# Performance work log

Measured on AMD Instinct MI355X. Metric: run time of the kernel, lower is better.

Reference implementation:

```python
import jax, jax.numpy as jnp
import numpy as np

N = 4096          # nodes per graph
F_IN = 256        # node_feature_dim
D_OUT = 128       # out_dim
E = N * N // 2    # edges per graph (so E1+E2 == N*N, required by .view(N, N))
NEG_SLOPE = 0.2   # PyG GATConv default negative_slope


def setup_inputs() -> dict:
    key = jax.random.key(0)
    k = jax.random.split(key, 7)
    x1 = jax.random.normal(k[0], (N, F_IN), dtype=jnp.float32)
    x2 = jax.random.normal(k[1], (N, F_IN), dtype=jnp.float32)
    edge_index1 = jax.random.randint(k[2], (2, E), 0, N, dtype=jnp.int64)
    edge_index2 = jax.random.randint(k[3], (2, E), 0, N, dtype=jnp.int64)
    W = jax.random.normal(k[4], (F_IN, D_OUT), dtype=jnp.float32) * 0.05
    att_src = jax.random.normal(k[5], (D_OUT,), dtype=jnp.float32) * 0.1
    att_dst = jax.random.normal(k[6], (D_OUT,), dtype=jnp.float32) * 0.1
    return {"x1": x1, "x2": x2, "edge_index1": edge_index1,
            "edge_index2": edge_index2, "W": W,
            "att_src": att_src, "att_dst": att_dst}


def reference(x1, x2, edge_index1, edge_index2, W, att_src, att_dst):
    n = x1.shape[0]
    # combine the two graphs into one block-diagonal graph (graph2 node ids shifted)
    x = jnp.concatenate([x1, x2], axis=0)                       # [2N, F]
    ei = jnp.concatenate([edge_index1, edge_index2 + n], axis=1)  # [2, N*N]
    src, dst = ei[0], ei[1]

    # GATConv (heads=1): linear transform then per-node logit halves
    h = x @ W                    # [2N, D]
    a_s = h @ att_src            # [2N]
    a_d = h @ att_dst            # [2N]

    # per-edge attention logits with leaky-relu
    e = jax.nn.leaky_relu(a_s[src] + a_d[dst], NEG_SLOPE)       # [N*N]

    # numerically-stable segment softmax grouped by destination node
    num_seg = 2 * n
    seg_max = jax.ops.segment_max(e, dst, num_segments=num_seg)
    ex = jnp.exp(e - seg_max[dst])
    denom = jax.ops.segment_sum(ex, dst, num_segments=num_seg)
    alpha = ex / denom[dst]                                     # [N*N]

    # forward returns only the attention weights reshaped to [N, N]
    return alpha.reshape(n, n)
```

## Files before the change

kernel.cpp:

```cpp
#include <hip/hip_runtime.h>


#define NNODES 4096
#define NSEG   8192
#define NEG_SLOPE 0.2f
#define EPB 32768

__global__ void k1_wvec(const float* __restrict__ W,
                        const float* __restrict__ att_src,
                        const float* __restrict__ att_dst,
                        float* __restrict__ wvs, float* __restrict__ wvd) {
    int f = threadIdx.x;
    const float* row = W + f * 128;
    float s = 0.f, d = 0.f;
    #pragma unroll 8
    for (int j = 0; j < 128; ++j) {
        float w = row[j];
        s += w * att_src[j];
        d += w * att_dst[j];
    }
    wvs[f] = s; wvd[f] = d;
}

__global__ void k2_logits(const float* __restrict__ x1, const float* __restrict__ x2,
                          const float* __restrict__ wvs, const float* __restrict__ wvd,
                          float* __restrict__ a_s, float* __restrict__ a_d) {
    int wave = blockIdx.x * 4 + (threadIdx.x >> 6);
    int lane = threadIdx.x & 63;
    const float* xrow = (wave < NNODES) ? (x1 + (size_t)wave * 256)
                                        : (x2 + (size_t)(wave - NNODES) * 256);
    float4 xv  = ((const float4*)xrow)[lane];
    float4 wsv = ((const float4*)wvs)[lane];
    float4 wdv = ((const float4*)wvd)[lane];
    float ps = xv.x*wsv.x + xv.y*wsv.y + xv.z*wsv.z + xv.w*wsv.w;
    float pd = xv.x*wdv.x + xv.y*wdv.y + xv.z*wdv.z + xv.w*wdv.w;
    #pragma unroll
    for (int o = 32; o > 0; o >>= 1) {
        ps += __shfl_down(ps, o);
        pd += __shfl_down(pd, o);
    }
    if (lane == 0) { a_s[wave] = ps; a_d[wave] = pd; }
}

__device__ __forceinline__ float lrelu_exp(float e) {
    e = (e > 0.f) ? e : NEG_SLOPE * e;
    return __expf(e);
}

__global__ __launch_bounds__(1024) void k3_denom(
        const int* __restrict__ ei1, const int* __restrict__ ei2,
        const float* __restrict__ a_s, const float* __restrict__ a_d,
        float* __restrict__ partials, int E1, int g1_blocks) {
    __shared__ float ssum[NNODES];
    __shared__ float las[NNODES];
    __shared__ float lad[NNODES];
    int t = threadIdx.x;
    int b = blockIdx.x;
    const int *sp, *dp; int nodeoff, qbase;
    if (b < g1_blocks) { sp = ei1; dp = ei1 + E1; nodeoff = 0;      qbase = b * (EPB/4); }
    else               { sp = ei2; dp = ei2 + E1; nodeoff = NNODES; qbase = (b - g1_blocks) * (EPB/4); }

    ((float4*)las)[t] = ((const float4*)(a_s + nodeoff))[t];
    ((float4*)lad)[t] = ((const float4*)(a_d + nodeoff))[t];
    for (int i = t; i < NNODES; i += 1024) ssum[i] = 0.f;
    __syncthreads();

    const int4* s4 = (const int4*)sp;
    const int4* d4 = (const int4*)dp;
    #pragma unroll
    for (int k = 0; k < 8; ++k) {
        int q = qbase + (k << 10) + t;
        int4 sv = s4[q];
        int4 dv = d4[q];
        float e0 = lrelu_exp(las[sv.x] + lad[dv.x]);
        float e1 = lrelu_exp(las[sv.y] + lad[dv.y]);
        float e2 = lrelu_exp(las[sv.z] + lad[dv.z]);
        float e3 = lrelu_exp(las[sv.w] + lad[dv.w]);
        atomicAdd(&ssum[dv.x], e0);
        atomicAdd(&ssum[dv.y], e1);
        atomicAdd(&ssum[dv.z], e2);
        atomicAdd(&ssum[dv.w], e3);
    }
    __syncthreads();
    float* pb = partials + (size_t)b * NNODES;
    for (int i = t; i < NNODES; i += 1024) pb[i] = ssum[i];
}

__global__ void k4a_reduce(const float* __restrict__ partials,
                           float* __restrict__ partials2, int g1_blocks) {
    int tid = blockIdx.x * blockDim.x + threadIdx.x;
    int c  = tid >> 13;
    int sg = tid & (NSEG - 1);
    int bpc = g1_blocks >> 3;
    int b0 = ((sg < NNODES) ? 0 : g1_blocks) + c * bpc;
    int col = sg & (NNODES - 1);
    float s = 0.f;
    for (int j = 0; j < bpc; ++j)
        s += partials[(size_t)(b0 + j) * NNODES + col];
    partials2[tid] = s;
}

__global__ void k4b_inv(const float* __restrict__ partials2,
                        float* __restrict__ inv_denom) {
    int sg = blockIdx.x * blockDim.x + threadIdx.x;
    float s = 0.f;
    #pragma unroll
    for (int c = 0; c < 8; ++c) s += partials2[c * NSEG + sg];
    inv_denom[sg] = 1.0f / s;
}

__global__ __launch_bounds__(1024) void k5_alpha(
        const int* __restrict__ ei1, const int* __restrict__ ei2,
        const float* __restrict__ a_s, const float* __restrict__ a_d,
        const float* __restrict__ inv_denom,
        float* __restrict__ out, int E1, int g1_blocks) {
    __shared__ float las[NNODES];
    __shared__ float lad[NNODES];
    __shared__ float linv[NNODES];
    int t = threadIdx.x;
    int b = blockIdx.x;
    const int *sp, *dp; int nodeoff, qbase, outbase;
    if (b < g1_blocks) { sp = ei1; dp = ei1 + E1; nodeoff = 0;      qbase = b * (EPB/4); outbase = 0; }
    else               { sp = ei2; dp = ei2 + E1; nodeoff = NNODES; qbase = (b - g1_blocks) * (EPB/4); outbase = E1 / 4; }

    ((float4*)las)[t]  = ((const float4*)(a_s + nodeoff))[t];
    ((float4*)lad)[t]  = ((const float4*)(a_d + nodeoff))[t];
    ((float4*)linv)[t] = ((const float4*)(inv_denom + nodeoff))[t];
    __syncthreads();

    const int4* s4 = (const int4*)sp;
    const int4* d4 = (const int4*)dp;
    float4* out4 = (float4*)out;
    #pragma unroll
    for (int k = 0; k < 8; ++k) {
        int q = qbase + (k << 10) + t;
        int4 sv = s4[q];
        int4 dv = d4[q];
        float4 r;
        r.x = lrelu_exp(las[sv.x] + lad[dv.x]) * linv[dv.x];
        r.y = lrelu_exp(las[sv.y] + lad[dv.y]) * linv[dv.y];
        r.z = lrelu_exp(las[sv.z] + lad[dv.z]) * linv[dv.z];
        r.w = lrelu_exp(las[sv.w] + lad[dv.w]) * linv[dv.w];
        out4[outbase + q] = r;
    }
}

extern "C" void kernel_launch(void* const* d_in, const int* in_sizes, int n_in,
                              void* d_out, int out_size, void* d_ws, size_t ws_size,
                              hipStream_t stream) {
    const float* x1      = (const float*)d_in[0];
    const float* x2      = (const float*)d_in[1];
    const int*   ei1     = (const int*)d_in[2];
    const int*   ei2     = (const int*)d_in[3];
    const float* W       = (const float*)d_in[4];
    const float* att_src = (const float*)d_in[5];
    const float* att_dst = (const float*)d_in[6];
    float* out = (float*)d_out;

    const int E1 = in_sizes[2] / 2;

    float* wsf       = (float*)d_ws;
    float* wvs       = wsf;
    float* wvd       = wsf + 256;
    float* a_s       = wsf + 512;
    float* a_d       = wsf + 512 + NSEG;
    float* inv_denom = wsf + 512 + 2*NSEG;
    float* partials2 = wsf + 32768;
    float* partials  = wsf + 131072;

    hipLaunchKernelGGL(k1_wvec, dim3(1), dim3(256), 0, stream,
                       W, att_src, att_dst, wvs, wvd);
    hipLaunchKernelGGL(k2_logits, dim3(2 * NNODES / 4), dim3(256), 0, stream,
                       x1, x2, wvs, wvd, a_s, a_d);

    int g1_blocks = E1 / EPB;
    hipLaunchKernelGGL(k3_denom, dim3(2 * g1_blocks), dim3(1024), 0, stream,
                       ei1, ei2, a_s, a_d, partials, E1, g1_blocks);
    hipLaunchKernelGGL(k4a_reduce, dim3(8 * NSEG / 256), dim3(256), 0, stream,
                       partials, partials2, g1_blocks);
    hipLaunchKernelGGL(k4b_inv, dim3(NSEG / 256), dim3(256), 0, stream,
                       partials2, inv_denom);

    hipLaunchKernelGGL(k5_alpha, dim3(2 * g1_blocks), dim3(1024), 0, stream,
                       ei1, ei2, a_s, a_d, inv_denom, out, E1, g1_blocks);
}
```

Baseline: 276.8 us.

## Replace LDS atomics with per-wave bins and tag-based conflict resolution

The denominator kernel now gives each wave its own private shared-memory histogram. Instead of LDS float atomics it writes a lane tag, and the lane that wins the tag does a plain add; after 8 retry rounds it falls back to an atomic. Both edge kernels also get smaller thread blocks and register double-buffered prefetch of the int4 edge indices. The aim is to avoid atomic contention and to hide global-load latency. In exchange, k3 now needs about 112KB of LDS per 256-thread block, which sharply limits occupancy, and each insert costs several extra LDS operations.

```diff
diff --git a/kernel.cpp b/kernel.cpp
--- a/kernel.cpp
+++ b/kernel.cpp
@@ -4,7 +4,11 @@
 #define NNODES 4096
 #define NSEG   8192
 #define NEG_SLOPE 0.2f
-#define EPB 32768
+
+#define K3_TPB 256
+#define K3_QPB 8192
+#define K5_TPB 512
+#define K5_QPB 8192
 
 __global__ void k1_wvec(const float* __restrict__ W,
                         const float* __restrict__ att_src,
@@ -47,43 +51,98 @@
     return __expf(e);
 }
 
-__global__ __launch_bounds__(1024) void k3_denom(
+__global__ __launch_bounds__(K3_TPB) void k3_denom(
         const int* __restrict__ ei1, const int* __restrict__ ei2,
         const float* __restrict__ a_s, const float* __restrict__ a_d,
         float* __restrict__ partials, int E1, int g1_blocks) {
-    __shared__ float ssum[NNODES];
+    __shared__ float bins[4][NNODES];
+    __shared__ int   tag[NNODES];
     __shared__ float las[NNODES];
     __shared__ float lad[NNODES];
+    volatile int* vtag = tag;
+
     int t = threadIdx.x;
+    float* binw = bins[t >> 6];
+
     int b = blockIdx.x;
-    const int *sp, *dp; int nodeoff, qbase;
-    if (b < g1_blocks) { sp = ei1; dp = ei1 + E1; nodeoff = 0;      qbase = b * (EPB/4); }
-    else               { sp = ei2; dp = ei2 + E1; nodeoff = NNODES; qbase = (b - g1_blocks) * (EPB/4); }
-
-    ((float4*)las)[t] = ((const float4*)(a_s + nodeoff))[t];
-    ((float4*)lad)[t] = ((const float4*)(a_d + nodeoff))[t];
-    for (int i = t; i < NNODES; i += 1024) ssum[i] = 0.f;
+    const int* sp; int qbase, nodeoff;
+    if (b < g1_blocks) { sp = ei1; qbase = b * K3_QPB; nodeoff = 0; }
+    else               { sp = ei2; qbase = (b - g1_blocks) * K3_QPB; nodeoff = NNODES; }
+    const int4* s4 = (const int4*)sp;
+    const int4* d4 = (const int4*)(sp + E1);
+
+    #pragma unroll
+    for (int i = 0; i < 4; ++i) {
+        ((float4*)las)[t + i*K3_TPB] = ((const float4*)(a_s + nodeoff))[t + i*K3_TPB];
+        ((float4*)lad)[t + i*K3_TPB] = ((const float4*)(a_d + nodeoff))[t + i*K3_TPB];
+    }
+    #pragma unroll
+    for (int i = 0; i < 16; ++i)
+        ((float4*)&bins[0][0])[t + i*K3_TPB] = make_float4(0.f,0.f,0.f,0.f);
     __syncthreads();
 
-    const int4* s4 = (const int4*)sp;
-    const int4* d4 = (const int4*)dp;
-    #pragma unroll
-    for (int k = 0; k < 8; ++k) {
-        int q = qbase + (k << 10) + t;
-        int4 sv = s4[q];
-        int4 dv = d4[q];
-        float e0 = lrelu_exp(las[sv.x] + lad[dv.x]);
-        float e1 = lrelu_exp(las[sv.y] + lad[dv.y]);
-        float e2 = lrelu_exp(las[sv.z] + lad[dv.z]);
-        float e3 = lrelu_exp(las[sv.w] + lad[dv.w]);
-        atomicAdd(&ssum[dv.x], e0);
-        atomicAdd(&ssum[dv.y], e1);
-        atomicAdd(&ssum[dv.z], e2);
-        atomicAdd(&ssum[dv.w], e3);
+    auto insert = [&](int d, float val) {
+        bool pending = true;
+        int rounds = 0;
+        while (__any(pending)) {
+            if (++rounds > 8) {
+                if (pending) atomicAdd(&binw[d], val);
+                break;
+            }
+            if (pending) vtag[d] = t;
+            if (pending && vtag[d] == t) {
+                binw[d] += val;
+                pending = false;
+            }
+        }
+    };
+
+    int4 sbuf[2][4], dbuf[2][4];
+    #pragma unroll
+    for (int i = 0; i < 4; ++i) {
+        int q = qbase + i*K3_TPB + t;
+        sbuf[0][i] = s4[q]; dbuf[0][i] = d4[q];
+    }
+    #pragma unroll
+    for (int bt = 0; bt < 8; ++bt) {
+        int cur = bt & 1, nxt = cur ^ 1;
+        if (bt < 7) {
+            #pragma unroll
+            for (int i = 0; i < 4; ++i) {
+                int q = qbase + ((bt+1)*4 + i)*K3_TPB + t;
+                sbuf[nxt][i] = s4[q]; dbuf[nxt][i] = d4[q];
+            }
+        }
+        #pragma unroll
+        for (int i = 0; i < 4; ++i) {
+            int4 sv = sbuf[cur][i], dv = dbuf[cur][i];
+            float e0 = las[sv.x] + lad[dv.x];
+            float e1 = las[sv.y] + lad[dv.y];
+            float e2 = las[sv.z] + lad[dv.z];
+            float e3 = las[sv.w] + lad[dv.w];
+            float v0 = lrelu_exp(e0), v1 = lrelu_exp(e1);
+            float v2 = lrelu_exp(e2), v3 = lrelu_exp(e3);
+            insert(dv.x, v0); insert(dv.y, v1);
+            insert(dv.z, v2); insert(dv.w, v3);
+        }
     }
     __syncthreads();
+
     float* pb = partials + (size_t)b * NNODES;
-    for (int i = t; i < NNODES; i += 1024) pb[i] = ssum[i];
+    #pragma unroll
+    for (int i = 0; i < 4; ++i) {
+        int c = t + i*K3_TPB;
+        float4 s0 = ((float4*)bins[0])[c];
+        float4 s1 = ((float4*)bins[1])[c];
+        float4 s2 = ((float4*)bins[2])[c];
+        float4 s3 = ((float4*)bins[3])[c];
+        float4 r;
+        r.x = s0.x+s1.x+s2.x+s3.x;
+        r.y = s0.y+s1.y+s2.y+s3.y;
+        r.z = s0.z+s1.z+s2.z+s3.z;
+        r.w = s0.w+s1.w+s2.w+s3.w;
+        ((float4*)pb)[c] = r;
+    }
 }
 
 __global__ void k4a_reduce(const float* __restrict__ partials,
@@ -109,7 +168,7 @@
     inv_denom[sg] = 1.0f / s;
 }
 
-__global__ __launch_bounds__(1024) void k5_alpha(
+__global__ __launch_bounds__(K5_TPB) void k5_alpha(
         const int* __restrict__ ei1, const int* __restrict__ ei2,
         const float* __restrict__ a_s, const float* __restrict__ a_d,
         const float* __restrict__ inv_denom,
@@ -119,29 +178,47 @@
     __shared__ float linv[NNODES];
     int t = threadIdx.x;
     int b = blockIdx.x;
-    const int *sp, *dp; int nodeoff, qbase, outbase;
-    if (b < g1_blocks) { sp = ei1; dp = ei1 + E1; nodeoff = 0;      qbase = b * (EPB/4); outbase = 0; }
-    else               { sp = ei2; dp = ei2 + E1; nodeoff = NNODES; qbase = (b - g1_blocks) * (EPB/4); outbase = E1 / 4; }
-
-    ((float4*)las)[t]  = ((const float4*)(a_s + nodeoff))[t];
-    ((float4*)lad)[t]  = ((const float4*)(a_d + nodeoff))[t];
-    ((float4*)linv)[t] = ((const float4*)(inv_denom + nodeoff))[t];
+    const int* sp; int qbase, outq, nodeoff;
+    if (b < g1_blocks) { sp = ei1; qbase = b * K5_QPB; outq = qbase; nodeoff = 0; }
+    else { sp = ei2; qbase = (b - g1_blocks) * K5_QPB; outq = E1/4 + qbase; nodeoff = NNODES; }
+    const int4* s4 = (const int4*)sp;
+    const int4* d4 = (const int4*)(sp + E1);
+
+    #pragma unroll
+    for (int i = 0; i < 2; ++i) {
+        ((float4*)las)[t + i*K5_TPB]  = ((const float4*)(a_s + nodeoff))[t + i*K5_TPB];
+        ((float4*)lad)[t + i*K5_TPB]  = ((const float4*)(a_d + nodeoff))[t + i*K5_TPB];
+        ((float4*)linv)[t + i*K5_TPB] = ((const float4*)(inv_denom + nodeoff))[t + i*K5_TPB];
+    }
     __syncthreads();
 
-    const int4* s4 = (const int4*)sp;
-    const int4* d4 = (const int4*)dp;
     float4* out4 = (float4*)out;
-    #pragma unroll
-    for (int k = 0; k < 8; ++k) {
-        int q = qbase + (k << 10) + t;
-        int4 sv = s4[q];
-        int4 dv = d4[q];
-        float4 r;
-        r.x = lrelu_exp(las[sv.x] + lad[dv.x]) * linv[dv.x];
-        r.y = lrelu_exp(las[sv.y] + lad[dv.y]) * linv[dv.y];
-        r.z = lrelu_exp(las[sv.z] + lad[dv.z]) * linv[dv.z];
-        r.w = lrelu_exp(las[sv.w] + lad[dv.w]) * linv[dv.w];
-        out4[outbase + q] = r;
+    int4 sbuf[2][4], dbuf[2][4];
+    #pragma unroll
+    for (int i = 0; i < 4; ++i) {
+        int q = qbase + i*K5_TPB + t;
+        sbuf[0][i] = s4[q]; dbuf[0][i] = d4[q];
+    }
+    #pragma unroll
+    for (int bt = 0; bt < 4; ++bt) {
+        int cur = bt & 1, nxt = cur ^ 1;
+        if (bt < 3) {
+            #pragma unroll
+            for (int i = 0; i < 4; ++i) {
+                int q = qbase + ((bt+1)*4 + i)*K5_TPB + t;
+                sbuf[nxt][i] = s4[q]; dbuf[nxt][i] = d4[q];
+            }
+        }
+        #pragma unroll
+        for (int i = 0; i < 4; ++i) {
+            int4 sv = sbuf[cur][i], dv = dbuf[cur][i];
+            float4 r;
+            r.x = lrelu_exp(las[sv.x] + lad[dv.x]) * linv[dv.x];
+            r.y = lrelu_exp(las[sv.y] + lad[dv.y]) * linv[dv.y];
+            r.z = lrelu_exp(las[sv.z] + lad[dv.z]) * linv[dv.z];
+            r.w = lrelu_exp(las[sv.w] + lad[dv.w]) * linv[dv.w];
+            out4[outq + (bt*4 + i)*K5_TPB + t] = r;
+        }
     }
 }
 
@@ -173,14 +250,15 @@
     hipLaunchKernelGGL(k2_logits, dim3(2 * NNODES / 4), dim3(256), 0, stream,
                        x1, x2, wvs, wvd, a_s, a_d);
 
-    int g1_blocks = E1 / EPB;
-    hipLaunchKernelGGL(k3_denom, dim3(2 * g1_blocks), dim3(1024), 0, stream,
-                       ei1, ei2, a_s, a_d, partials, E1, g1_blocks);
+    int g1b3 = (E1 / 4) / K3_QPB;
+    hipLaunchKernelGGL(k3_denom, dim3(2 * g1b3), dim3(K3_TPB), 0, stream,
+                       ei1, ei2, a_s, a_d, partials, E1, g1b3);
     hipLaunchKernelGGL(k4a_reduce, dim3(8 * NSEG / 256), dim3(256), 0, stream,
-                       partials, partials2, g1_blocks);
+                       partials, partials2, g1b3);
     hipLaunchKernelGGL(k4b_inv, dim3(NSEG / 256), dim3(256), 0, stream,
                        partials2, inv_denom);
 
-    hipLaunchKernelGGL(k5_alpha, dim3(2 * g1_blocks), dim3(1024), 0, stream,
-                       ei1, ei2, a_s, a_d, inv_denom, out, E1, g1_blocks);
-}
+    int g1b5 = (E1 / 4) / K5_QPB;
+    hipLaunchKernelGGL(k5_alpha, dim3(2 * g1b5), dim3(K5_TPB), 0, stream,
+                       ei1, ei2, a_s, a_d, inv_denom, out, E1, g1b5);
+}
```

New measurement: 298.5 us. 7.8% more time.

## Store exp values in denom pass and rescale them in alpha pass

Applied to the files above, without the earlier changes.

The denominator kernel now writes the unnormalized exp values straight into the output buffer. The alpha kernel then only reads dst indices and those stored values and multiplies by the inverse denominator. This drops the src index read and the exp recompute from the second pass, at the cost of an extra output write plus read of the same size. The a_d table is now read from global memory instead of being staged in shared memory, which shrinks LDS use per block.

```diff
diff --git a/kernel.cpp b/kernel.cpp
--- a/kernel.cpp
+++ b/kernel.cpp
@@ -4,7 +4,8 @@
 #define NNODES 4096
 #define NSEG   8192
 #define NEG_SLOPE 0.2f
-#define EPB 32768
+#define EK_TPB 1024
+#define EK_QPB 8192
 
 __global__ void k1_wvec(const float* __restrict__ W,
                         const float* __restrict__ att_src,
@@ -47,43 +48,46 @@
     return __expf(e);
 }
 
-__global__ __launch_bounds__(1024) void k3_denom(
+__global__ __launch_bounds__(EK_TPB) void k3_denom(
         const int* __restrict__ ei1, const int* __restrict__ ei2,
         const float* __restrict__ a_s, const float* __restrict__ a_d,
-        float* __restrict__ partials, int E1, int g1_blocks) {
+        float* __restrict__ partials, float* __restrict__ out,
+        int E1, int g1_blocks) {
     __shared__ float ssum[NNODES];
     __shared__ float las[NNODES];
-    __shared__ float lad[NNODES];
     int t = threadIdx.x;
     int b = blockIdx.x;
-    const int *sp, *dp; int nodeoff, qbase;
-    if (b < g1_blocks) { sp = ei1; dp = ei1 + E1; nodeoff = 0;      qbase = b * (EPB/4); }
-    else               { sp = ei2; dp = ei2 + E1; nodeoff = NNODES; qbase = (b - g1_blocks) * (EPB/4); }
+    const int* sp; int qbase, nodeoff, outq;
+    if (b < g1_blocks) { sp = ei1; qbase = b * EK_QPB; nodeoff = 0; outq = qbase; }
+    else { sp = ei2; qbase = (b - g1_blocks) * EK_QPB; nodeoff = NNODES; outq = E1/4 + qbase; }
+    const int4* s4 = (const int4*)sp;
+    const int4* d4 = (const int4*)(sp + E1);
+    const float* adg = a_d + nodeoff;
 
-    ((float4*)las)[t] = ((const float4*)(a_s + nodeoff))[t];
-    ((float4*)lad)[t] = ((const float4*)(a_d + nodeoff))[t];
-    for (int i = t; i < NNODES; i += 1024) ssum[i] = 0.f;
+    ((float4*)las)[t]  = ((const float4*)(a_s + nodeoff))[t];
+    ((float4*)ssum)[t] = make_float4(0.f, 0.f, 0.f, 0.f);
     __syncthreads();
 
-    const int4* s4 = (const int4*)sp;
-    const int4* d4 = (const int4*)dp;
+    float4* out4 = (float4*)out;
     #pragma unroll
     for (int k = 0; k < 8; ++k) {
         int q = qbase + (k << 10) + t;
         int4 sv = s4[q];
         int4 dv = d4[q];
-        float e0 = lrelu_exp(las[sv.x] + lad[dv.x]);
-        float e1 = lrelu_exp(las[sv.y] + lad[dv.y]);
-        float e2 = lrelu_exp(las[sv.z] + lad[dv.z]);
-        float e3 = lrelu_exp(las[sv.w] + lad[dv.w]);
+        float ad0 = adg[dv.x], ad1 = adg[dv.y], ad2 = adg[dv.z], ad3 = adg[dv.w];
+        float e0 = lrelu_exp(las[sv.x] + ad0);
+        float e1 = lrelu_exp(las[sv.y] + ad1);
+        float e2 = lrelu_exp(las[sv.z] + ad2);
+        float e3 = lrelu_exp(las[sv.w] + ad3);
         atomicAdd(&ssum[dv.x], e0);
         atomicAdd(&ssum[dv.y], e1);
         atomicAdd(&ssum[dv.z], e2);
         atomicAdd(&ssum[dv.w], e3);
+        out4[outq + (k << 10) + t] = make_float4(e0, e1, e2, e3);
     }
     __syncthreads();
     float* pb = partials + (size_t)b * NNODES;
-    for (int i = t; i < NNODES; i += 1024) pb[i] = ssum[i];
+    ((float4*)pb)[t] = ((float4*)ssum)[t];
 }
 
 __global__ void k4a_reduce(const float* __restrict__ partials,
@@ -109,39 +113,32 @@
     inv_denom[sg] = 1.0f / s;
 }
 
-__global__ __launch_bounds__(1024) void k5_alpha(
+__global__ __launch_bounds__(EK_TPB) void k5_alpha(
         const int* __restrict__ ei1, const int* __restrict__ ei2,
-        const float* __restrict__ a_s, const float* __restrict__ a_d,
         const float* __restrict__ inv_denom,
         float* __restrict__ out, int E1, int g1_blocks) {
-    __shared__ float las[NNODES];
-    __shared__ float lad[NNODES];
     __shared__ float linv[NNODES];
     int t = threadIdx.x;
     int b = blockIdx.x;
-    const int *sp, *dp; int nodeoff, qbase, outbase;
-    if (b < g1_blocks) { sp = ei1; dp = ei1 + E1; nodeoff = 0;      qbase = b * (EPB/4); outbase = 0; }
-    else               { sp = ei2; dp = ei2 + E1; nodeoff = NNODES; qbase = (b - g1_blocks) * (EPB/4); outbase = E1 / 4; }
+    const int* sp; int qbase, nodeoff, outq;
+    if (b < g1_blocks) { sp = ei1; qbase = b * EK_QPB; nodeoff = 0; outq = qbase; }
+    else { sp = ei2; qbase = (b - g1_blocks) * EK_QPB; nodeoff = NNODES; outq = E1/4 + qbase; }
+    const int4* d4 = (const int4*)(sp + E1);
 
-    ((float4*)las)[t]  = ((const float4*)(a_s + nodeoff))[t];
-    ((float4*)lad)[t]  = ((const float4*)(a_d + nodeoff))[t];
     ((float4*)linv)[t] = ((const float4*)(inv_denom + nodeoff))[t];
     __syncthreads();
 
-    const int4* s4 = (const int4*)sp;
-    const int4* d4 = (const int4*)dp;
     float4* out4 = (float4*)out;
     #pragma unroll
     for (int k = 0; k < 8; ++k) {
         int q = qbase + (k << 10) + t;
-        int4 sv = s4[q];
-        int4 dv = d4[q];
-        float4 r;
-        r.x = lrelu_exp(las[sv.x] + lad[dv.x]) * linv[dv.x];
-        r.y = lrelu_exp(las[sv.y] + lad[dv.y]) * linv[dv.y];
-        r.z = lrelu_exp(las[sv.z] + lad[dv.z]) * linv[dv.z];
-        r.w = lrelu_exp(las[sv.w] + lad[dv.w]) * linv[dv.w];
-        out4[outbase + q] = r;
+        int4  dv = d4[q];
+        float4 ex = out4[outq + (k << 10) + t];
+        ex.x *= linv[dv.x];
+        ex.y *= linv[dv.y];
+        ex.z *= linv[dv.z];
+        ex.w *= linv[dv.w];
+        out4[outq + (k << 10) + t] = ex;
     }
 }
 
@@ -173,14 +170,13 @@
     hipLaunchKernelGGL(k2_logits, dim3(2 * NNODES / 4), dim3(256), 0, stream,
                        x1, x2, wvs, wvd, a_s, a_d);
 
-    int g1_blocks = E1 / EPB;
-    hipLaunchKernelGGL(k3_denom, dim3(2 * g1_blocks), dim3(1024), 0, stream,
-                       ei1, ei2, a_s, a_d, partials, E1, g1_blocks);
+    int g1b = (E1 / 4) / EK_QPB;
+    hipLaunchKernelGGL(k3_denom, dim3(2 * g1b), dim3(EK_TPB), 0, stream,
+                       ei1, ei2, a_s, a_d, partials, out, E1, g1b);
     hipLaunchKernelGGL(k4a_reduce, dim3(8 * NSEG / 256), dim3(256), 0, stream,
-                       partials, partials2, g1_blocks);
+                       partials, partials2, g1b);
     hipLaunchKernelGGL(k4b_inv, dim3(NSEG / 256), dim3(256), 0, stream,
                        partials2, inv_denom);
-
-    hipLaunchKernelGGL(k5_alpha, dim3(2 * g1_blocks), dim3(1024), 0, stream,
-                       ei1, ei2, a_s, a_d, inv_denom, out, E1, g1_blocks);
+    hipLaunchKernelGGL(k5_alpha, dim3(2 * g1b), dim3(EK_TPB), 0, stream,
+                       ei1, ei2, inv_denom, out, E1, g1b);
 }
```

After: 271.7 us. Within noise of the previous version (-1.8%).
